# Kernel optimization log

Hardware: AMD Instinct MI355X
Metric: run time of the kernel (lower is better)

Reference implementation:

```python
import jax, jax.numpy as jnp
import numpy as np

N_NODES = 100000
N_EDGES = 1600000
D_IN = 64
H = 64


def setup_inputs() -> dict:
    key = jax.random.key(0)
    ks = jax.random.split(key, 8)
    inp = {
        "x": jax.random.normal(ks[0], (N_NODES, D_IN), dtype=jnp.float32),
        "edge_index": jax.random.randint(ks[1], (2, N_EDGES), 0, N_NODES, dtype=jnp.int64),
        # layer 1 (SAGEConv): lin_l (aggregated neighbors, with bias), lin_r (root, no bias)
        "Wl1": jax.random.normal(ks[2], (D_IN, H), dtype=jnp.float32) / np.sqrt(D_IN),
        "bl1": jnp.zeros((H,), dtype=jnp.float32),
        "Wr1": jax.random.normal(ks[3], (D_IN, H), dtype=jnp.float32) / np.sqrt(D_IN),
        # layer 2
        "Wl2": jax.random.normal(ks[4], (H, H), dtype=jnp.float32) / np.sqrt(H),
        "bl2": jnp.zeros((H,), dtype=jnp.float32),
        "Wr2": jax.random.normal(ks[5], (H, H), dtype=jnp.float32) / np.sqrt(H),
        "Wfc": jax.random.normal(ks[6], (H, 1), dtype=jnp.float32) / np.sqrt(H),
        "bfc": jnp.zeros((1,), dtype=jnp.float32),
    }
    return inp


def _sage_conv(h, src, dst, inv_deg, Wl, bl, Wr):
    # mean-aggregate neighbor features: scatter-add messages then normalize by in-degree
    agg = jax.ops.segment_sum(h[src], dst, num_segments=N_NODES)  # [N, d]
    agg = agg * inv_deg[:, None]
    return agg @ Wl + bl + h @ Wr


def reference(x, edge_index, Wl1, bl1, Wr1, Wl2, bl2, Wr2, Wfc, bfc):
    src, dst = edge_index[0], edge_index[1]
    deg = jax.ops.segment_sum(jnp.ones((src.shape[0],), dtype=x.dtype), dst,
                              num_segments=N_NODES)
    inv_deg = jnp.where(deg > 0, 1.0 / jnp.maximum(deg, 1.0), 0.0)

    h = jax.nn.relu(_sage_conv(x, src, dst, inv_deg, Wl1, bl1, Wr1))
    h = jax.nn.relu(_sage_conv(h, src, dst, inv_deg, Wl2, bl2, Wr2))
    return h @ Wfc + bfc  # [N, 1]
```

## Files before the change

kernel.cpp:

```cpp
#include <hip/hip_runtime.h>
#include <hip/hip_fp16.h>

#define NN 100000
#define NE 1600000
#define SHIFT 8
#define NBUCK 391
#define P1B   391
#define EPB   4093

typedef _Float16 f16x8 __attribute__((ext_vector_type(8)));
typedef float f32x4 __attribute__((ext_vector_type(4)));
union H8U4 { f16x8 h; uint4 u; };

__device__ __forceinline__ int scan256(int* s, int t, int v) {
    s[t] = v;
    __syncthreads();
    for (int off = 1; off < 256; off <<= 1) {
        int add = (t >= off) ? s[t - off] : 0;
        __syncthreads();
        s[t] += add;
        __syncthreads();
    }
    return s[t];
}

__global__ __launch_bounds__(256) void k_hist(
    const float4* __restrict__ x4, ushort4* __restrict__ xh4,
    const float* __restrict__ Wl1, const float* __restrict__ Wr1, unsigned short* __restrict__ wt1,
    const float* __restrict__ Wl2, const float* __restrict__ Wr2, unsigned short* __restrict__ wt2,
    const int* __restrict__ dst, int* __restrict__ hist, int* __restrict__ bin_total)
{
    __shared__ int h[NBUCK];
    int t = threadIdx.x, blk = blockIdx.x;

    const int n4 = NN * 16;
    const int per = (n4 + P1B - 1) / P1B;
    int cb = blk * per, ce = min(cb + per, n4);
    for (int i = cb + t; i < ce; i += 256) {
        float4 f = x4[i];
        _Float16 a = (_Float16)f.x, b = (_Float16)f.y, c = (_Float16)f.z, d = (_Float16)f.w;
        ushort4 u;
        u.x = *(unsigned short*)&a; u.y = *(unsigned short*)&b;
        u.z = *(unsigned short*)&c; u.w = *(unsigned short*)&d;
        xh4[i] = u;
    }
    if (blk < 64) {
        int idx = (blk & 31) * 256 + t;
        const float* Wl = (blk < 32) ? Wl1 : Wl2;
        const float* Wr = (blk < 32) ? Wr1 : Wr2;
        unsigned short* wt = (blk < 32) ? wt1 : wt2;
        int n = idx >> 7, k = idx & 127;
        float v = (k < 64) ? Wl[k * 64 + n] : Wr[(k - 64) * 64 + n];
        _Float16 hv = (_Float16)v;
        wt[idx] = *(unsigned short*)&hv;
    }

    for (int i = t; i < NBUCK; i += 256) h[i] = 0;
    __syncthreads();
    int eb = blk * EPB, ee = min(eb + EPB, NE);
    for (int e = eb + t; e < ee; e += 256) atomicAdd(&h[dst[e] >> SHIFT], 1);
    __syncthreads();
    for (int i = t; i < NBUCK; i += 256) {
        int v = h[i];
        hist[(size_t)i * P1B + blk] = v;
        if (v) atomicAdd(&bin_total[i], v);
    }
}

__global__ __launch_bounds__(256) void k_cursor(int* __restrict__ hist, const int* __restrict__ bin_total,
                                                int* __restrict__ bucket_start, int* __restrict__ offsets) {
    __shared__ int sS[256];
    int b = blockIdx.x, t = threadIdx.x;

    int v = 0;
    for (int i = t; i < b; i += 256) v += bin_total[i];
    sS[t] = v;
    __syncthreads();
    for (int s = 128; s > 0; s >>= 1) {
        if (t < s) sS[t] += sS[t + s];
        __syncthreads();
    }
    int base = sS[0];
    __syncthreads();
    if (t == 0) bucket_start[b] = base;
    if (b == 0 && t == 0) { bucket_start[NBUCK] = NE; offsets[NN] = NE; }

    int carry = 0;
#pragma unroll
    for (int c = 0; c < 2; c++) {
        int idx = c * 256 + t;
        int hv = (idx < P1B) ? hist[(size_t)b * P1B + idx] : 0;
        int incl = scan256(sS, t, hv);
        if (idx < P1B) hist[(size_t)b * P1B + idx] = base + carry + incl - hv;
        __syncthreads();
        carry += sS[255];
        __syncthreads();
    }
}

__global__ __launch_bounds__(256) void k_scatter(const int* __restrict__ src, const int* __restrict__ dst,
                                                 const int* __restrict__ hist, unsigned int* __restrict__ pairs) {
    __shared__ int cur[NBUCK];
    int t = threadIdx.x, blk = blockIdx.x;
    for (int i = t; i < NBUCK; i += 256) cur[i] = hist[(size_t)i * P1B + blk];
    __syncthreads();
    int eb = blk * EPB, ee = min(eb + EPB, NE);
    for (int e = eb + t; e < ee; e += 256) {
        int d = dst[e];
        int pos = atomicAdd(&cur[d >> SHIFT], 1);
        pairs[pos] = (unsigned int)src[e] | ((unsigned int)(d & 255) << 17);
    }
}

__global__ __launch_bounds__(256) void k_bucket_csr(const unsigned int* __restrict__ pairs,
                                                    const int* __restrict__ bucket_start,
                                                    int* __restrict__ ssrc, int* __restrict__ offsets,
                                                    float* __restrict__ inv_deg) {
    __shared__ int cnt[256];
    __shared__ int sS[256];
    int b = blockIdx.x, t = threadIdx.x;
    cnt[t] = 0;
    __syncthreads();
    int beg = bucket_start[b], end = bucket_start[b + 1];
    for (int e = beg + t; e < end; e += 256) atomicAdd(&cnt[pairs[e] >> 17], 1);
    __syncthreads();
    int deg = cnt[t];
    int incl = scan256(sS, t, deg);
    int ex = incl - deg;
    int node = (b << SHIFT) + t;
    if (node < NN) {
        offsets[node] = beg + ex;
        inv_deg[node] = (deg > 0) ? (1.0f / (float)deg) : 0.0f;
    }
    __syncthreads();
    cnt[t] = beg + ex;
    __syncthreads();
    for (int e = beg + t; e < end; e += 256) {
        unsigned int pr = pairs[e];
        int pos = atomicAdd(&cnt[pr >> 17], 1);
        ssrc[pos] = (int)(pr & 0x1FFFFu);
    }
}

__device__ __forceinline__ void agg_pair(const uint4* __restrict__ featq, const int* __restrict__ ssrc,
                                         int beg0, int end0, int beg1, int end1,
                                         int c, int g, H8U4& acc0, H8U4& acc1) {
    int e0 = beg0, e1 = beg1;

    while (e0 + 16 <= end0 && e1 + 16 <= end1) {
        int i00 = ssrc[e0 + g], i01 = ssrc[e0 + 8 + g];
        int i10 = ssrc[e1 + g], i11 = ssrc[e1 + 8 + g];
        H8U4 q00, q01, q10, q11;
        q00.u = featq[(size_t)i00 * 8 + c];
        q01.u = featq[(size_t)i01 * 8 + c];
        q10.u = featq[(size_t)i10 * 8 + c];
        q11.u = featq[(size_t)i11 * 8 + c];
        acc0.h += q00.h; acc0.h += q01.h;
        acc1.h += q10.h; acc1.h += q11.h;
        e0 += 16; e1 += 16;
    }
    for (; e0 + 16 <= end0; e0 += 16) {
        int i0 = ssrc[e0 + g], i1 = ssrc[e0 + 8 + g];
        H8U4 q0, q1;
        q0.u = featq[(size_t)i0 * 8 + c];
        q1.u = featq[(size_t)i1 * 8 + c];
        acc0.h += q0.h; acc0.h += q1.h;
    }
    for (; e0 < end0; e0 += 8) {
        int m = end0 - e0;
        int idx = ssrc[e0 + (g < m ? g : m - 1)];
        H8U4 q;
        q.u = featq[(size_t)idx * 8 + c];
        if (g < m) acc0.h += q.h;
    }
    for (; e1 + 16 <= end1; e1 += 16) {
        int i0 = ssrc[e1 + g], i1 = ssrc[e1 + 8 + g];
        H8U4 q0, q1;
        q0.u = featq[(size_t)i0 * 8 + c];
        q1.u = featq[(size_t)i1 * 8 + c];
        acc1.h += q0.h; acc1.h += q1.h;
    }
    for (; e1 < end1; e1 += 8) {
        int m = end1 - e1;
        int idx = ssrc[e1 + (g < m ? g : m - 1)];
        H8U4 q;
        q.u = featq[(size_t)idx * 8 + c];
        if (g < m) acc1.h += q.h;
    }
}

template <bool FUSE_HEAD>
__global__ __launch_bounds__(256) void k_fused(const uint4* __restrict__ featq,
                                               const int* __restrict__ ssrc,
                                               const int* __restrict__ offsets, const float* __restrict__ inv_deg,
                                               const uint4* __restrict__ wtq,
                                               const float* __restrict__ bias,
                                               const float* __restrict__ Wfc, const float* __restrict__ bfc,
                                               float* __restrict__ out_f32, unsigned short* __restrict__ out_f16) {
    __shared__ uint4 sAgg[32][9];

    int tid = threadIdx.x;
    int wave = tid >> 6, lane = tid & 63;
    int base = blockIdx.x * 32;

    {
        int c = lane & 7, g = lane >> 3;
#pragma unroll 1
        for (int p = 0; p < 4; ++p) {
            int l0 = wave * 8 + p * 2;
            int node0 = base + l0;
            int node1 = node0 + 1;
            if (node0 >= NN) {
                if (g == 0) {
                    uint4 z = {0u, 0u, 0u, 0u};
                    sAgg[l0][c] = z;
                    sAgg[l0 + 1][c] = z;
                }
                continue;
            }
            bool has1 = node1 < NN;
            int beg0 = offsets[node0], end0 = offsets[node0 + 1];
            int beg1 = has1 ? offsets[node1] : 0, end1 = has1 ? offsets[node1 + 1] : 0;
            H8U4 acc0, acc1;
            acc0.h = (f16x8)(_Float16)0;
            acc1.h = (f16x8)(_Float16)0;
            agg_pair(featq, ssrc, beg0, end0, beg1, end1, c, g, acc0, acc1);

#pragma unroll
            for (int mask = 8; mask <= 32; mask <<= 1) {
                H8U4 o0, o1;
                o0.u.x = __shfl_xor(acc0.u.x, mask); o0.u.y = __shfl_xor(acc0.u.y, mask);
                o0.u.z = __shfl_xor(acc0.u.z, mask); o0.u.w = __shfl_xor(acc0.u.w, mask);
                o1.u.x = __shfl_xor(acc1.u.x, mask); o1.u.y = __shfl_xor(acc1.u.y, mask);
                o1.u.z = __shfl_xor(acc1.u.z, mask); o1.u.w = __shfl_xor(acc1.u.w, mask);
                acc0.h += o0.h;
                acc1.h += o1.h;
            }

            if (g == 0) {
                float s0 = inv_deg[node0];
                H8U4 r;
#pragma unroll
                for (int j = 0; j < 8; j++) r.h[j] = (_Float16)((float)acc0.h[j] * s0);
                sAgg[l0][c] = r.u;
                H8U4 r1;
                if (has1) {
                    float s1 = inv_deg[node1];
#pragma unroll
                    for (int j = 0; j < 8; j++) r1.h[j] = (_Float16)((float)acc1.h[j] * s1);
                } else {
                    r1.u = (uint4){0u, 0u, 0u, 0u};
                }
                sAgg[l0 + 1][c] = r1.u;
            }
        }
    }
    __syncthreads();

    if (wave >= 2) return;

    int nb = base + wave * 16;
    int m = lane & 15, quad = lane >> 4;
    int l = wave * 16 + m;

    int an = nb + m;
    if (an > NN - 1) an = NN - 1;
    H8U4 a[4];
    a[0].u = sAgg[l][quad];
    a[1].u = sAgg[l][4 + quad];
    a[2].u = featq[(size_t)an * 8 + quad];
    a[3].u = featq[(size_t)an * 8 + 4 + quad];

    f32x4 acc[4];
#pragma unroll
    for (int n = 0; n < 4; n++) acc[n] = (f32x4){0.f, 0.f, 0.f, 0.f};

#pragma unroll
    for (int ncol = 0; ncol < 4; ncol++) {
        int col = ncol * 16 + m;
#pragma unroll
        for (int ki = 0; ki < 4; ki++) {
            H8U4 b;
            b.u = wtq[col * 16 + ki * 4 + quad];
            acc[ncol] = __builtin_amdgcn_mfma_f32_16x16x32_f16(a[ki].h, b.h, acc[ncol], 0, 0, 0);
        }
    }

    float bs[4];
#pragma unroll
    for (int ncol = 0; ncol < 4; ncol++) bs[ncol] = bias[ncol * 16 + m];

    if (!FUSE_HEAD) {
#pragma unroll
        for (int r = 0; r < 4; r++) {
            int node = nb + quad * 4 + r;
            if (node < NN) {
#pragma unroll
                for (int ncol = 0; ncol < 4; ncol++) {
                    float v = fmaxf(acc[ncol][r] + bs[ncol], 0.f);
                    _Float16 hv = (_Float16)v;
                    out_f16[(size_t)node * 64 + ncol * 16 + m] = *(unsigned short*)&hv;
                }
            }
        }
    } else {
        float wf[4];
#pragma unroll
        for (int ncol = 0; ncol < 4; ncol++) wf[ncol] = Wfc[ncol * 16 + m];
#pragma unroll
        for (int r = 0; r < 4; r++) {
            int node = nb + quad * 4 + r;
            float partial = 0.f;
#pragma unroll
            for (int ncol = 0; ncol < 4; ncol++)
                partial += fmaxf(acc[ncol][r] + bs[ncol], 0.f) * wf[ncol];
            partial += __shfl_xor(partial, 1);
            partial += __shfl_xor(partial, 2);
            partial += __shfl_xor(partial, 4);
            partial += __shfl_xor(partial, 8);
            if (m == 0 && node < NN) out_f32[node] = partial + bfc[0];
        }
    }
}

extern "C" void kernel_launch(void* const* d_in, const int* in_sizes, int n_in,
                              void* d_out, int out_size, void* d_ws, size_t ws_size,
                              hipStream_t stream) {
    const float* x   = (const float*)d_in[0];
    const int*   ei  = (const int*)d_in[1];
    const float* Wl1 = (const float*)d_in[2];
    const float* bl1 = (const float*)d_in[3];
    const float* Wr1 = (const float*)d_in[4];
    const float* Wl2 = (const float*)d_in[5];
    const float* bl2 = (const float*)d_in[6];
    const float* Wr2 = (const float*)d_in[7];
    const float* Wfc = (const float*)d_in[8];
    const float* bfc = (const float*)d_in[9];
    float* out = (float*)d_out;

    const int* srcp = ei;
    const int* dstp = ei + NE;

    char* p = (char*)d_ws;
    auto carve = [&](size_t bytes) {
        char* q = p;
        p += (bytes + 255) & ~size_t(255);
        return q;
    };
    int*            offsets = (int*)carve((size_t)(NN + 1) * 4);
    float*          inv_deg = (float*)carve((size_t)NN * 4);
    int*            ssrc    = (int*)carve((size_t)NE * 4);
    unsigned short* xh      = (unsigned short*)carve((size_t)NN * 64 * 2);
    unsigned short* h1h     = (unsigned short*)carve((size_t)NN * 64 * 2);
    unsigned short* wt1     = (unsigned short*)carve(64 * 128 * 2);
    unsigned short* wt2     = (unsigned short*)carve(64 * 128 * 2);
    unsigned int*   pairs   = (unsigned int*)carve((size_t)NE * 4);
    int*            hist    = (int*)carve((size_t)NBUCK * P1B * 4);
    int*            bin_total    = (int*)carve((size_t)NBUCK * 4);
    int*            bucket_start = (int*)carve((size_t)(NBUCK + 1) * 4);

    const int tile = (NN + 31) / 32;

    hipMemsetAsync(bin_total, 0, NBUCK * 4, stream);
    k_hist<<<P1B, 256, 0, stream>>>((const float4*)x, (ushort4*)xh,
                                    Wl1, Wr1, wt1, Wl2, Wr2, wt2, dstp, hist, bin_total);
    k_cursor<<<NBUCK, 256, 0, stream>>>(hist, bin_total, bucket_start, offsets);
    k_scatter<<<P1B, 256, 0, stream>>>(srcp, dstp, hist, pairs);
    k_bucket_csr<<<NBUCK, 256, 0, stream>>>(pairs, bucket_start, ssrc, offsets, inv_deg);

    k_fused<false><<<tile, 256, 0, stream>>>((const uint4*)xh, ssrc, offsets, inv_deg,
                                             (const uint4*)wt1, bl1, Wfc, bfc, nullptr, h1h);
    k_fused<true><<<tile, 256, 0, stream>>>((const uint4*)h1h, ssrc, offsets, inv_deg,
                                            (const uint4*)wt2, bl2, Wfc, bfc, out, nullptr);
}
```

Baseline: 244.8 us.

## Use finer 64-node buckets and split the cursor scan into row and bin scans

Shrinks the counting-sort buckets from 256 to 64 nodes, which gives 1563 buckets, and raises the histogram and scatter block count to 1024. The old single cursor kernel, which relied on global atomics plus a per-block prefix over bin totals, is replaced by a per-row scan kernel and a single-block scan over bins. The per-bucket CSR step now uses a wavefront shuffle scan in place of a block-wide shared-memory scan. The aim is more parallelism and cheaper per-bucket work, at the cost of one extra launch, a larger hist array, and a serial single-block bin scan.

New measurement: 254.0 us. 1.04x slower.

```diff
diff --git a/kernel.cpp b/kernel.cpp
--- a/kernel.cpp
+++ b/kernel.cpp
@@ -3,10 +3,10 @@
 
 #define NN 100000
 #define NE 1600000
-#define SHIFT 8
-#define NBUCK 391
-#define P1B   391
-#define EPB   4093
+#define SHIFT 6
+#define NBUCK 1563
+#define P1B   1024
+#define EPB   1563
 
 typedef _Float16 f16x8 __attribute__((ext_vector_type(8)));
 typedef float f32x4 __attribute__((ext_vector_type(4)));
@@ -28,7 +28,7 @@
     const float4* __restrict__ x4, ushort4* __restrict__ xh4,
     const float* __restrict__ Wl1, const float* __restrict__ Wr1, unsigned short* __restrict__ wt1,
     const float* __restrict__ Wl2, const float* __restrict__ Wr2, unsigned short* __restrict__ wt2,
-    const int* __restrict__ dst, int* __restrict__ hist, int* __restrict__ bin_total)
+    const int* __restrict__ dst, int* __restrict__ hist)
 {
     __shared__ int h[NBUCK];
     int t = threadIdx.x, blk = blockIdx.x;
@@ -60,55 +60,53 @@
     int eb = blk * EPB, ee = min(eb + EPB, NE);
     for (int e = eb + t; e < ee; e += 256) atomicAdd(&h[dst[e] >> SHIFT], 1);
     __syncthreads();
-    for (int i = t; i < NBUCK; i += 256) {
-        int v = h[i];
-        hist[(size_t)i * P1B + blk] = v;
-        if (v) atomicAdd(&bin_total[i], v);
-    }
-}
-
-__global__ __launch_bounds__(256) void k_cursor(int* __restrict__ hist, const int* __restrict__ bin_total,
-                                                int* __restrict__ bucket_start, int* __restrict__ offsets) {
+    for (int i = t; i < NBUCK; i += 256) hist[(size_t)i * P1B + blk] = h[i];
+}
+
+__global__ __launch_bounds__(256) void k_rowscan(int* __restrict__ hist, int* __restrict__ row_total) {
     __shared__ int sS[256];
     int b = blockIdx.x, t = threadIdx.x;
-
-    int v = 0;
-    for (int i = t; i < b; i += 256) v += bin_total[i];
-    sS[t] = v;
-    __syncthreads();
-    for (int s = 128; s > 0; s >>= 1) {
-        if (t < s) sS[t] += sS[t + s];
-        __syncthreads();
-    }
-    int base = sS[0];
-    __syncthreads();
-    if (t == 0) bucket_start[b] = base;
-    if (b == 0 && t == 0) { bucket_start[NBUCK] = NE; offsets[NN] = NE; }
-
+    int4 v = ((int4*)(hist + (size_t)b * P1B))[t];
+    int s = v.x + v.y + v.z + v.w;
+    int incl = scan256(sS, t, s);
+    int ex = incl - s;
+    int4 w;
+    w.x = ex; w.y = ex + v.x; w.z = w.y + v.y; w.w = w.z + v.z;
+    ((int4*)(hist + (size_t)b * P1B))[t] = w;
+    if (t == 255) row_total[b] = incl;
+}
+
+__global__ __launch_bounds__(256) void k_binscan(const int* __restrict__ row_total,
+                                                 int* __restrict__ bucket_start, int* __restrict__ offsets) {
+    __shared__ int sS[256];
+    int t = threadIdx.x;
     int carry = 0;
 #pragma unroll
-    for (int c = 0; c < 2; c++) {
+    for (int c = 0; c < 7; c++) {
         int idx = c * 256 + t;
-        int hv = (idx < P1B) ? hist[(size_t)b * P1B + idx] : 0;
-        int incl = scan256(sS, t, hv);
-        if (idx < P1B) hist[(size_t)b * P1B + idx] = base + carry + incl - hv;
+        int v = (idx < NBUCK) ? row_total[idx] : 0;
+        int incl = scan256(sS, t, v);
+        if (idx < NBUCK) bucket_start[idx] = carry + incl - v;
         __syncthreads();
         carry += sS[255];
         __syncthreads();
     }
+    if (t == 0) { bucket_start[NBUCK] = NE; offsets[NN] = NE; }
 }
 
 __global__ __launch_bounds__(256) void k_scatter(const int* __restrict__ src, const int* __restrict__ dst,
-                                                 const int* __restrict__ hist, unsigned int* __restrict__ pairs) {
+                                                 const int* __restrict__ hist, const int* __restrict__ bucket_start,
+                                                 unsigned int* __restrict__ pairs) {
     __shared__ int cur[NBUCK];
     int t = threadIdx.x, blk = blockIdx.x;
-    for (int i = t; i < NBUCK; i += 256) cur[i] = hist[(size_t)i * P1B + blk];
+    for (int i = t; i < NBUCK; i += 256)
+        cur[i] = bucket_start[i] + hist[(size_t)i * P1B + blk];
     __syncthreads();
     int eb = blk * EPB, ee = min(eb + EPB, NE);
     for (int e = eb + t; e < ee; e += 256) {
         int d = dst[e];
         int pos = atomicAdd(&cur[d >> SHIFT], 1);
-        pairs[pos] = (unsigned int)src[e] | ((unsigned int)(d & 255) << 17);
+        pairs[pos] = (unsigned int)src[e] | ((unsigned int)(d & 63) << 17);
     }
 }
 
@@ -116,28 +114,34 @@
                                                     const int* __restrict__ bucket_start,
                                                     int* __restrict__ ssrc, int* __restrict__ offsets,
                                                     float* __restrict__ inv_deg) {
-    __shared__ int cnt[256];
-    __shared__ int sS[256];
+    __shared__ int cnt[64];
+    __shared__ int cur[64];
     int b = blockIdx.x, t = threadIdx.x;
-    cnt[t] = 0;
+    if (t < 64) cnt[t] = 0;
     __syncthreads();
     int beg = bucket_start[b], end = bucket_start[b + 1];
     for (int e = beg + t; e < end; e += 256) atomicAdd(&cnt[pairs[e] >> 17], 1);
     __syncthreads();
-    int deg = cnt[t];
-    int incl = scan256(sS, t, deg);
-    int ex = incl - deg;
-    int node = (b << SHIFT) + t;
-    if (node < NN) {
-        offsets[node] = beg + ex;
-        inv_deg[node] = (deg > 0) ? (1.0f / (float)deg) : 0.0f;
-    }
-    __syncthreads();
-    cnt[t] = beg + ex;
+    if (t < 64) {
+        int deg = cnt[t];
+        int incl = deg;
+#pragma unroll
+        for (int s = 1; s < 64; s <<= 1) {
+            int v = __shfl_up(incl, s);
+            if (t >= s) incl += v;
+        }
+        int ex = incl - deg;
+        int node = (b << SHIFT) + t;
+        if (node < NN) {
+            offsets[node] = beg + ex;
+            inv_deg[node] = (deg > 0) ? (1.0f / (float)deg) : 0.0f;
+        }
+        cur[t] = beg + ex;
+    }
     __syncthreads();
     for (int e = beg + t; e < end; e += 256) {
         unsigned int pr = pairs[e];
-        int pos = atomicAdd(&cnt[pr >> 17], 1);
+        int pos = atomicAdd(&cur[pr >> 17], 1);
         ssrc[pos] = (int)(pr & 0x1FFFFu);
     }
 }
@@ -356,16 +360,16 @@
     unsigned short* wt2     = (unsigned short*)carve(64 * 128 * 2);
     unsigned int*   pairs   = (unsigned int*)carve((size_t)NE * 4);
     int*            hist    = (int*)carve((size_t)NBUCK * P1B * 4);
-    int*            bin_total    = (int*)carve((size_t)NBUCK * 4);
+    int*            row_total    = (int*)carve((size_t)NBUCK * 4);
     int*            bucket_start = (int*)carve((size_t)(NBUCK + 1) * 4);
 
     const int tile = (NN + 31) / 32;
 
-    hipMemsetAsync(bin_total, 0, NBUCK * 4, stream);
     k_hist<<<P1B, 256, 0, stream>>>((const float4*)x, (ushort4*)xh,
-                                    Wl1, Wr1, wt1, Wl2, Wr2, wt2, dstp, hist, bin_total);
-    k_cursor<<<NBUCK, 256, 0, stream>>>(hist, bin_total, bucket_start, offsets);
-    k_scatter<<<P1B, 256, 0, stream>>>(srcp, dstp, hist, pairs);
+                                    Wl1, Wr1, wt1, Wl2, Wr2, wt2, dstp, hist);
+    k_rowscan<<<NBUCK, 256, 0, stream>>>(hist, row_total);
+    k_binscan<<<1, 256, 0, stream>>>(row_total, bucket_start, offsets);
+    k_scatter<<<P1B, 256, 0, stream>>>(srcp, dstp, hist, bucket_start, pairs);
     k_bucket_csr<<<NBUCK, 256, 0, stream>>>(pairs, bucket_start, ssrc, offsets, inv_deg);
 
     k_fused<false><<<tile, 256, 0, stream>>>((const uint4*)xh, ssrc, offsets, inv_deg,
```

## Restructure edge bucketing: more histogram blocks, column scan, drop global atomics

Applied to the files above, without the earlier changes.

Raises the number of histogram/scatter blocks from 391 to 1024 with fewer edges each, and stores the per-block histogram row-major. The cursor kernel becomes a per-bucket column scan over the 1024 block counts. The bucket-level exclusive prefix is now recomputed inside the scatter and CSR kernels, which removes the global atomic bin totals and the memset. This aims to improve GPU occupancy and parallelism in the preprocessing stages, in exchange for redundant small scans in each block and strided column reads.

Result: no change. 245.0 us (+0.1%).

```diff
diff --git a/kernel.cpp b/kernel.cpp
--- a/kernel.cpp
+++ b/kernel.cpp
@@ -5,8 +5,8 @@
 #define NE 1600000
 #define SHIFT 8
 #define NBUCK 391
-#define P1B   391
-#define EPB   4093
+#define P1B   1024
+#define EPB   1563
 
 typedef _Float16 f16x8 __attribute__((ext_vector_type(8)));
 typedef float f32x4 __attribute__((ext_vector_type(4)));
@@ -28,7 +28,7 @@
     const float4* __restrict__ x4, ushort4* __restrict__ xh4,
     const float* __restrict__ Wl1, const float* __restrict__ Wr1, unsigned short* __restrict__ wt1,
     const float* __restrict__ Wl2, const float* __restrict__ Wr2, unsigned short* __restrict__ wt2,
-    const int* __restrict__ dst, int* __restrict__ hist, int* __restrict__ bin_total)
+    const int* __restrict__ dst, int* __restrict__ hist)
 {
     __shared__ int h[NBUCK];
     int t = threadIdx.x, blk = blockIdx.x;
@@ -60,50 +60,46 @@
     int eb = blk * EPB, ee = min(eb + EPB, NE);
     for (int e = eb + t; e < ee; e += 256) atomicAdd(&h[dst[e] >> SHIFT], 1);
     __syncthreads();
-    for (int i = t; i < NBUCK; i += 256) {
-        int v = h[i];
-        hist[(size_t)i * P1B + blk] = v;
-        if (v) atomicAdd(&bin_total[i], v);
-    }
-}
-
-__global__ __launch_bounds__(256) void k_cursor(int* __restrict__ hist, const int* __restrict__ bin_total,
-                                                int* __restrict__ bucket_start, int* __restrict__ offsets) {
+    for (int i = t; i < NBUCK; i += 256) hist[(size_t)blk * NBUCK + i] = h[i];
+}
+
+__global__ __launch_bounds__(256) void k_colscan(int* __restrict__ hist, int* __restrict__ total,
+                                                 int* __restrict__ offsets) {
     __shared__ int sS[256];
     int b = blockIdx.x, t = threadIdx.x;
-
-    int v = 0;
-    for (int i = t; i < b; i += 256) v += bin_total[i];
-    sS[t] = v;
-    __syncthreads();
-    for (int s = 128; s > 0; s >>= 1) {
-        if (t < s) sS[t] += sS[t + s];
-        __syncthreads();
-    }
-    int base = sS[0];
-    __syncthreads();
-    if (t == 0) bucket_start[b] = base;
-    if (b == 0 && t == 0) { bucket_start[NBUCK] = NE; offsets[NN] = NE; }
-
+    int v0 = hist[(size_t)(t * 4 + 0) * NBUCK + b];
+    int v1 = hist[(size_t)(t * 4 + 1) * NBUCK + b];
+    int v2 = hist[(size_t)(t * 4 + 2) * NBUCK + b];
+    int v3 = hist[(size_t)(t * 4 + 3) * NBUCK + b];
+    int s = v0 + v1 + v2 + v3;
+    int incl = scan256(sS, t, s);
+    int ex = incl - s;
+    hist[(size_t)(t * 4 + 0) * NBUCK + b] = ex;
+    hist[(size_t)(t * 4 + 1) * NBUCK + b] = ex + v0;
+    hist[(size_t)(t * 4 + 2) * NBUCK + b] = ex + v0 + v1;
+    hist[(size_t)(t * 4 + 3) * NBUCK + b] = ex + v0 + v1 + v2;
+    if (t == 255) total[b] = incl;
+    if (b == 0 && t == 0) offsets[NN] = NE;
+}
+
+__global__ __launch_bounds__(256) void k_scatter(const int* __restrict__ src, const int* __restrict__ dst,
+                                                 const int* __restrict__ hist, const int* __restrict__ total,
+                                                 unsigned int* __restrict__ pairs) {
+    __shared__ int cur[NBUCK];
+    __shared__ int sS[256];
+    int t = threadIdx.x, blk = blockIdx.x;
     int carry = 0;
 #pragma unroll
     for (int c = 0; c < 2; c++) {
         int idx = c * 256 + t;
-        int hv = (idx < P1B) ? hist[(size_t)b * P1B + idx] : 0;
-        int incl = scan256(sS, t, hv);
-        if (idx < P1B) hist[(size_t)b * P1B + idx] = base + carry + incl - hv;
+        int v = (idx < NBUCK) ? total[idx] : 0;
+        int incl = scan256(sS, t, v);
+        if (idx < NBUCK)
+            cur[idx] = carry + incl - v + hist[(size_t)blk * NBUCK + idx];
         __syncthreads();
         carry += sS[255];
         __syncthreads();
     }
-}
-
-__global__ __launch_bounds__(256) void k_scatter(const int* __restrict__ src, const int* __restrict__ dst,
-                                                 const int* __restrict__ hist, unsigned int* __restrict__ pairs) {
-    __shared__ int cur[NBUCK];
-    int t = threadIdx.x, blk = blockIdx.x;
-    for (int i = t; i < NBUCK; i += 256) cur[i] = hist[(size_t)i * P1B + blk];
-    __syncthreads();
     int eb = blk * EPB, ee = min(eb + EPB, NE);
     for (int e = eb + t; e < ee; e += 256) {
         int d = dst[e];
@@ -113,15 +109,25 @@
 }
 
 __global__ __launch_bounds__(256) void k_bucket_csr(const unsigned int* __restrict__ pairs,
-                                                    const int* __restrict__ bucket_start,
+                                                    const int* __restrict__ total,
                                                     int* __restrict__ ssrc, int* __restrict__ offsets,
                                                     float* __restrict__ inv_deg) {
     __shared__ int cnt[256];
     __shared__ int sS[256];
     int b = blockIdx.x, t = threadIdx.x;
+    int v = 0;
+    for (int i = t; i < b; i += 256) v += total[i];
+    sS[t] = v;
+    __syncthreads();
+    for (int s = 128; s > 0; s >>= 1) {
+        if (t < s) sS[t] += sS[t + s];
+        __syncthreads();
+    }
+    int beg = sS[0];
+    int end = beg + total[b];
+    __syncthreads();
     cnt[t] = 0;
     __syncthreads();
-    int beg = bucket_start[b], end = bucket_start[b + 1];
     for (int e = beg + t; e < end; e += 256) atomicAdd(&cnt[pairs[e] >> 17], 1);
     __syncthreads();
     int deg = cnt[t];
@@ -355,18 +361,16 @@
     unsigned short* wt1     = (unsigned short*)carve(64 * 128 * 2);
     unsigned short* wt2     = (unsigned short*)carve(64 * 128 * 2);
     unsigned int*   pairs   = (unsigned int*)carve((size_t)NE * 4);
-    int*            hist    = (int*)carve((size_t)NBUCK * P1B * 4);
-    int*            bin_total    = (int*)carve((size_t)NBUCK * 4);
-    int*            bucket_start = (int*)carve((size_t)(NBUCK + 1) * 4);
+    int*            hist    = (int*)carve((size_t)P1B * NBUCK * 4);
+    int*            total   = (int*)carve((size_t)NBUCK * 4);
 
     const int tile = (NN + 31) / 32;
 
-    hipMemsetAsync(bin_total, 0, NBUCK * 4, stream);
     k_hist<<<P1B, 256, 0, stream>>>((const float4*)x, (ushort4*)xh,
-                                    Wl1, Wr1, wt1, Wl2, Wr2, wt2, dstp, hist, bin_total);
-    k_cursor<<<NBUCK, 256, 0, stream>>>(hist, bin_total, bucket_start, offsets);
-    k_scatter<<<P1B, 256, 0, stream>>>(srcp, dstp, hist, pairs);
-    k_bucket_csr<<<NBUCK, 256, 0, stream>>>(pairs, bucket_start, ssrc, offsets, inv_deg);
+                                    Wl1, Wr1, wt1, Wl2, Wr2, wt2, dstp, hist);
+    k_colscan<<<NBUCK, 256, 0, stream>>>(hist, total, offsets);
+    k_scatter<<<P1B, 256, 0, stream>>>(srcp, dstp, hist, total, pairs);
+    k_bucket_csr<<<NBUCK, 256, 0, stream>>>(pairs, total, ssrc, offsets, inv_deg);
 
     k_fused<false><<<tile, 256, 0, stream>>>((const uint4*)xh, ssrc, offsets, inv_deg,
                                              (const uint4*)wt1, bl1, Wfc, bfc, nullptr, h1h);
```
